# Kernel optimization log

Measured on AMD Instinct MI355X. Metric: run time of the kernel, lower is better.

## Reference

```python
import jax, jax.numpy as jnp
import numpy as np

B, LS, LL = 1024, 128, 2048
E, VOCAB = 16, 160000
NH, KD = 8, 6
LSH_DIM, TOPK = 16, 48
D_ITEM = 3 * E  # 48
EPS = 1e-3  # keras LayerNormalization default epsilon


def setup_inputs() -> dict:
    key = jax.random.key(0)
    ks = iter(jax.random.split(key, 64))
    def nk():
        return next(ks)
    def ids(shape):
        return jax.random.randint(nk(), shape, 0, VOCAB, dtype=jnp.int32)
    inp = {}
    for n in ['uid', 'utag1', 'utag2', 'utag3', 'utag4',
              'label_goods_ids', 'label_shop_ids', 'label_cate_ids']:
        inp[n] = ids((B,))
    for n in ['shortterm_goods_ids', 'shortterm_shop_ids', 'shortterm_cate_ids']:
        inp[n] = ids((B, LS))
    for n in ['longterm_goods_ids', 'longterm_shop_ids', 'longterm_cate_ids']:
        inp[n] = ids((B, LL))
    def rn(shape, s=0.05):
        return (jax.random.normal(nk(), shape) * s).astype(jnp.float32)
    inp['emb_table'] = rn((VOCAB, E))
    inp['H'] = rn((D_ITEM, LSH_DIM), 1.0)  # non-trainable random projection
    for p in ('s', 'l'):
        inp[p + 'Wq'] = rn((D_ITEM, NH, KD)); inp[p + 'bq'] = jnp.zeros((NH, KD), jnp.float32)
        inp[p + 'Wk'] = rn((D_ITEM, NH, KD)); inp[p + 'bk'] = jnp.zeros((NH, KD), jnp.float32)
        inp[p + 'Wv'] = rn((D_ITEM, NH, KD)); inp[p + 'bv'] = jnp.zeros((NH, KD), jnp.float32)
        inp[p + 'Wo'] = rn((NH, KD, D_ITEM)); inp[p + 'bo'] = jnp.zeros((D_ITEM,), jnp.float32)
    Din = D_ITEM + 5 * E + D_ITEM + D_ITEM  # 224
    inp['W1'] = rn((Din, 200)); inp['b1'] = jnp.zeros((200,), jnp.float32)
    inp['g1'] = jnp.ones((200,), jnp.float32); inp['be1'] = jnp.zeros((200,), jnp.float32)
    inp['W2'] = rn((200, 80)); inp['b2'] = jnp.zeros((80,), jnp.float32)
    inp['g2'] = jnp.ones((80,), jnp.float32); inp['be2'] = jnp.zeros((80,), jnp.float32)
    inp['W3'] = rn((80, 1)); inp['b3'] = jnp.zeros((1,), jnp.float32)
    return inp


def _ln(x, g, b):
    m = jnp.mean(x, axis=-1, keepdims=True)
    v = jnp.mean((x - m) ** 2, axis=-1, keepdims=True)
    return (x - m) * jax.lax.rsqrt(v + EPS) * g + b


def _mha(q, kv, mask3, Wq, bq, Wk, bk, Wv, bv, Wo, bo):
    # q: [B,1,D], kv: [B,K,D], mask3: [B,1,K] float (1=keep)
    qh = jnp.einsum('bqe,ehd->bqhd', q, Wq) + bq
    kh = jnp.einsum('bke,ehd->bkhd', kv, Wk) + bk
    vh = jnp.einsum('bke,ehd->bkhd', kv, Wv) + bv
    sc = jnp.einsum('bqhd,bkhd->bhqk', qh, kh) / jnp.sqrt(jnp.float32(KD))
    sc = sc + (1.0 - mask3[:, None, :, :]) * jnp.float32(-1e9)
    a = jax.nn.softmax(sc, axis=-1)
    o = jnp.einsum('bhqk,bkhd->bqhd', a, vh)
    return jnp.einsum('bqhd,hde->bqe', o, Wo) + bo


def reference(uid, utag1, utag2, utag3, utag4,
              label_goods_ids, label_shop_ids, label_cate_ids,
              shortterm_goods_ids, shortterm_shop_ids, shortterm_cate_ids,
              longterm_goods_ids, longterm_shop_ids, longterm_cate_ids,
              emb_table, H,
              sWq, sbq, sWk, sbk, sWv, sbv, sWo, sbo,
              lWq, lbq, lWk, lbk, lWv, lbv, lWo, lbo,
              W1, b1, g1, be1, W2, b2, g2, be2, W3, b3):
    short_mask = shortterm_goods_ids == 0  # padding_index == 0
    long_mask = longterm_goods_ids == 0

    def stack_embed(lst):
        X = jnp.stack([t if t.ndim == 2 else t[:, None] for t in lst], axis=2)  # [B,L,F]
        Xe = emb_table[X]  # [B,L,F,E]
        return Xe.reshape(Xe.shape[0], Xe.shape[1], -1)

    X_item = stack_embed([label_goods_ids, label_shop_ids, label_cate_ids])  # [B,1,48]
    X_user = stack_embed([uid, utag1, utag2, utag3, utag4])                  # [B,1,80]
    X_short = stack_embed([shortterm_goods_ids, shortterm_shop_ids, shortterm_cate_ids])  # [B,LS,48]
    X_long = stack_embed([longterm_goods_ids, longterm_shop_ids, longterm_cate_ids])      # [B,LL,48]

    # short-term interest
    slen = jnp.sum((~short_mask).astype(jnp.int32), axis=1)
    smask = (jnp.arange(LS)[None, :] < slen[:, None]).astype(jnp.float32)[:, None, :]
    short_int = _mha(X_item, X_short, smask, sWq, sbq, sWk, sbk, sWv, sbv, sWo, sbo)[:, 0]

    # long-term interest: LSH sign-hash hamming top-k retrieval
    series_codes = jnp.sign(jnp.einsum('ble,em->blm', X_long, H))  # [B,LL,16]
    item_codes = jnp.sign(jnp.einsum('ble,em->blm', X_item, H))    # [B,1,16]
    scores = jnp.sum((series_codes == item_codes).astype(jnp.float32), axis=-1)  # [B,LL]
    scores = jnp.where(long_mask, -jnp.inf, scores)
    _, idx = jax.lax.top_k(scores, TOPK)  # descending, padded entries last
    top_emb = jnp.take_along_axis(X_long, idx[:, :, None], axis=1)  # [B,TOPK,48]
    top_mask = jnp.take_along_axis(long_mask, idx, axis=1)
    llen = jnp.sum((~top_mask).astype(jnp.int32), axis=1)
    lmask = (jnp.arange(TOPK)[None, :] < llen[:, None]).astype(jnp.float32)[:, None, :]
    long_int = _mha(X_item, top_emb, lmask, lWq, lbq, lWk, lbk, lWv, lbv, lWo, lbo)[:, 0]

    x = jnp.concatenate([X_item[:, 0], X_user[:, 0], short_int, long_int], axis=1)  # [B,224]
    h1 = jax.nn.relu(_ln(x @ W1 + b1, g1, be1))
    h2 = jax.nn.relu(_ln(h1 @ W2 + b2, g2, be2))
    out = jax.nn.sigmoid(h2 @ W3 + b3)  # [B,1]
    return out
```

## Files before the change

kernel.cpp:

```cpp
#include <hip/hip_runtime.h>
#include <hip/hip_fp16.h>
#include <math.h>

#define BB 1024
#define LSx 128
#define LLx 2048
#define TOPKx 48
#define VOCABx 160000

__global__ __launch_bounds__(256) void k_partial(
    const float* __restrict__ emb, const float* __restrict__ Hm,
    __half* __restrict__ Ph)
{
  const int idx = blockIdx.x * 256 + threadIdx.x;
  if (idx >= VOCABx * 48) return;
  const int v = idx / 48;
  const int r = idx - v * 48;
  const int seg = r >> 4, m = r & 15;
  const float* er = emb + (size_t)v * 16;
  float a = 0.f;
  #pragma unroll
  for (int e = 0; e < 16; ++e) a += er[e] * Hm[(seg * 16 + e) * 16 + m];
  Ph[idx] = __float2half(a);
}

__global__ __launch_bounds__(512) void k_score_topk(
    const int* __restrict__ lg, const int* __restrict__ lsh, const int* __restrict__ lc,
    const int* __restrict__ ig, const int* __restrict__ ish, const int* __restrict__ ici,
    const float* __restrict__ emb, const float* __restrict__ Hm,
    const __half* __restrict__ Ph,
    int* __restrict__ sel)
{
  __shared__ int idsL[3 * LLx];
  __shared__ signed char scores[LLx];
  __shared__ float Xitem[48];
  __shared__ int icodeS[16];
  __shared__ int hist[18];
  __shared__ int cnt_above;
  __shared__ int wsum[8];
  const int b = blockIdx.x, tid = threadIdx.x;

  ((int4*)idsL)[tid]        = ((const int4*)(lg  + (size_t)b * LLx))[tid];
  ((int4*)idsL)[512 + tid]  = ((const int4*)(lsh + (size_t)b * LLx))[tid];
  ((int4*)idsL)[1024 + tid] = ((const int4*)(lc  + (size_t)b * LLx))[tid];
  if (tid < 48) {
    const int seg = tid >> 4, e = tid & 15;
    const int id = (seg == 0) ? ig[b] : (seg == 1) ? ish[b] : ici[b];
    Xitem[tid] = emb[(size_t)id * 16 + e];
  }
  if (tid < 18) hist[tid] = 0;
  if (tid == 0) cnt_above = 0;
  __syncthreads();
  if (tid < 16) {
    float dd = 0.f;
    for (int e = 0; e < 48; ++e) dd += Xitem[e] * Hm[e * 16 + tid];
    icodeS[tid] = (dd > 0.f) ? 1 : (dd < 0.f ? -1 : 0);
  }
  __syncthreads();

  const int l16 = tid & 15;
  const int grpw = (tid >> 4) & 3;
  const int grp32 = tid >> 4;
  const int myic = icodeS[l16];

  for (int r4 = 0; r4 < 64; r4 += 4) {
    int g_[4], s_[4], c_[4];
    #pragma unroll
    for (int u = 0; u < 4; ++u) {
      const int p = (r4 + u) * 32 + grp32;
      g_[u] = idsL[p]; s_[u] = idsL[LLx + p]; c_[u] = idsL[2 * LLx + p];
    }
    float d0[4], d1[4], d2[4];
    #pragma unroll
    for (int u = 0; u < 4; ++u) {
      d0[u] = __half2float(Ph[(size_t)g_[u] * 48 + l16]);
      d1[u] = __half2float(Ph[(size_t)s_[u] * 48 + 16 + l16]);
      d2[u] = __half2float(Ph[(size_t)c_[u] * 48 + 32 + l16]);
    }
    #pragma unroll
    for (int u = 0; u < 4; ++u) {
      const int p = (r4 + u) * 32 + grp32;
      const float d = (d0[u] + d1[u]) + d2[u];
      const int cs = (d > 0.f) ? 1 : (d < 0.f ? -1 : 0);
      const unsigned long long bal = __ballot(cs == myic);
      int sc = (int)__popcll((bal >> (16 * grpw)) & 0xFFFFull);
      if (g_[u] == 0) sc = -1;
      if (l16 == 0) {
        scores[p] = (signed char)sc;
        atomicAdd(&hist[sc + 1], 1);
      }
    }
  }
  __syncthreads();

  int above = 0, tval = -1, need = 0;
  for (int s = 16; s >= -1; --s) {
    const int c = hist[s + 1];
    if (above + c >= TOPKx) { tval = s; need = TOPKx - above; break; }
    above += c;
  }

  const int base_l = tid * 4;
  int myscore[4];
  #pragma unroll
  for (int j = 0; j < 4; ++j) myscore[j] = scores[base_l + j];
  int cnt = 0;
  #pragma unroll
  for (int j = 0; j < 4; ++j) cnt += (myscore[j] == tval) ? 1 : 0;
  int v = cnt;
  const int lane = tid & 63, wave = tid >> 6;
  #pragma unroll
  for (int o = 1; o < 64; o <<= 1) {
    const int u = __shfl_up(v, o, 64);
    if (lane >= o) v += u;
  }
  if (lane == 63) wsum[wave] = v;
  __syncthreads();
  int rank = v - cnt;
  for (int w = 0; w < wave; ++w) rank += wsum[w];

  #pragma unroll
  for (int j = 0; j < 4; ++j) {
    const int l = base_l + j;
    const int s = myscore[j];
    if (s > tval) {
      const int slot = atomicAdd(&cnt_above, 1);
      sel[b * TOPKx + slot] = l;
    } else if (s == tval) {
      if (rank < need) sel[b * TOPKx + above + rank] = l;
      ++rank;
    }
  }
}

__device__ __forceinline__ void kv_accum(
    const float* __restrict__ W, const float* __restrict__ bvec,
    int gid, int sid, int cid, const float* __restrict__ emb, float acc[48])
{
  #pragma unroll
  for (int j = 0; j < 48; ++j) acc[j] = bvec[j];
  const int ids3[3] = {gid, sid, cid};
  #pragma unroll
  for (int seg = 0; seg < 3; ++seg) {
    const float* row = emb + (size_t)ids3[seg] * 16;
    #pragma unroll
    for (int i4 = 0; i4 < 4; ++i4) {
      const float4 xv = ((const float4*)row)[i4];
      const float xs[4] = {xv.x, xv.y, xv.z, xv.w};
      #pragma unroll
      for (int c = 0; c < 4; ++c) {
        const int e = seg * 16 + i4 * 4 + c;
        const float* wr = W + e * 48;
        const float xe = xs[c];
        #pragma unroll
        for (int j = 0; j < 48; ++j) acc[j] += xe * wr[j];
      }
    }
  }
}

template<int K, int STRIDE, bool IS_LONG>
__global__ __launch_bounds__(256) void k_mha(
    const int* __restrict__ kg, const int* __restrict__ ks, const int* __restrict__ kc,
    const int* __restrict__ ig, const int* __restrict__ ish, const int* __restrict__ ici,
    const float* __restrict__ emb,
    const float* __restrict__ Wq, const float* __restrict__ bq,
    const float* __restrict__ Wk, const float* __restrict__ bk,
    const float* __restrict__ Wv, const float* __restrict__ bv,
    const float* __restrict__ Wo, const float* __restrict__ bo,
    const int* __restrict__ sel,
    float* __restrict__ outv)
{
  __shared__ float Xitem[48];
  __shared__ float qh[48];
  __shared__ __align__(16) float vhs[K][48];
  __shared__ float scs[8][K + 4];
  __shared__ float osm[48];
  __shared__ unsigned char validf[K];
  const int b = blockIdx.x, tid = threadIdx.x;
  const int role = tid >> 7;
  const int p = tid & 127;

  if (tid < 48) {
    const int seg = tid >> 4, e = tid & 15;
    const int id = (seg == 0) ? ig[b] : (seg == 1) ? ish[b] : ici[b];
    Xitem[tid] = emb[(size_t)id * 16 + e];
  }
  __syncthreads();
  if (tid < 48) {
    float a = bq[tid];
    for (int e = 0; e < 48; ++e) a += Xitem[e] * Wq[e * 48 + tid];
    qh[tid] = a;
  }

  int gid = 0, sid = 0, cid = 0;
  if (p < K) {
    const int pos = IS_LONG ? sel[b * TOPKx + p] : p;
    const size_t off = (size_t)b * STRIDE + pos;
    gid = kg[off]; sid = ks[off]; cid = kc[off];
  }
  const int nval = __syncthreads_count(role == 0 && p < K && gid != 0);

  if (p < K) {
    if (role == 0) {
      float acc[48];
      kv_accum(Wk, bk, gid, sid, cid, emb, acc);
      validf[p] = IS_LONG ? (unsigned char)(gid != 0) : (unsigned char)(p < nval);
      #pragma unroll
      for (int h = 0; h < 8; ++h) {
        float s = 0.f;
        #pragma unroll
        for (int d = 0; d < 6; ++d) s += qh[h * 6 + d] * acc[h * 6 + d];
        scs[h][p] = s * 0.40824829046386301637f;
      }
    } else {
      float acc[48];
      kv_accum(Wv, bv, gid, sid, cid, emb, acc);
      #pragma unroll
      for (int j = 0; j < 48; ++j) vhs[p][j] = acc[j];
    }
  }
  __syncthreads();

  if (tid < 128) {
    const int h = tid >> 4, l16 = tid & 15;
    float amax = -INFINITY;
    for (int k = l16; k < K; k += 16) if (validf[k]) amax = fmaxf(amax, scs[h][k]);
    #pragma unroll
    for (int m = 1; m < 16; m <<= 1) amax = fmaxf(amax, __shfl_xor(amax, m, 16));
    if (nval == 0) {
      for (int k = l16; k < K; k += 16) scs[h][k] = 1.0f / (float)K;
    } else {
      float ssum = 0.f;
      for (int k = l16; k < K; k += 16) {
        const float ev = validf[k] ? expf(scs[h][k] - amax) : 0.f;
        scs[h][k] = ev;
        ssum += ev;
      }
      #pragma unroll
      for (int m = 1; m < 16; m <<= 1) ssum += __shfl_xor(ssum, m, 16);
      const float inv = 1.0f / ssum;
      for (int k = l16; k < K; k += 16) scs[h][k] *= inv;
    }
  }
  __syncthreads();

  if (tid < 48) {
    const int h = tid / 6;
    float a = 0.f;
    for (int k = 0; k < K; ++k) a += scs[h][k] * vhs[k][tid];
    osm[tid] = a;
  }
  __syncthreads();
  if (tid < 48) {
    float r = bo[tid];
    for (int j = 0; j < 48; ++j) r += osm[j] * Wo[j * 48 + tid];
    outv[b * 48 + tid] = r;
  }
}

__device__ __forceinline__ float block_sum256(float v, float* red) {
  #pragma unroll
  for (int m = 32; m >= 1; m >>= 1) v += __shfl_xor(v, m, 64);
  const int lane = threadIdx.x & 63, wave = threadIdx.x >> 6;
  if (lane == 0) red[wave] = v;
  __syncthreads();
  const float t = red[0] + red[1] + red[2] + red[3];
  __syncthreads();
  return t;
}

__global__ __launch_bounds__(256) void k_mlp(
    const int* __restrict__ uid, const int* __restrict__ u1, const int* __restrict__ u2,
    const int* __restrict__ u3, const int* __restrict__ u4,
    const int* __restrict__ ig, const int* __restrict__ ish, const int* __restrict__ ici,
    const float* __restrict__ emb,
    const float* __restrict__ sint, const float* __restrict__ lint,
    const float* __restrict__ W1, const float* __restrict__ b1,
    const float* __restrict__ g1, const float* __restrict__ be1,
    const float* __restrict__ W2, const float* __restrict__ b2,
    const float* __restrict__ g2, const float* __restrict__ be2,
    const float* __restrict__ W3, const float* __restrict__ b3,
    float* __restrict__ out)
{
  __shared__ __align__(16) float x[224];
  __shared__ __align__(16) float h1[200];
  __shared__ float h2[80];
  __shared__ float red[4];
  const int b = blockIdx.x, tid = threadIdx.x;

  if (tid < 128) {
    const int e = tid & 15;
    int id;
    if (tid < 48) {
      const int seg = tid >> 4;
      id = (seg == 0) ? ig[b] : (seg == 1) ? ish[b] : ici[b];
    } else {
      const int f = (tid - 48) >> 4;
      id = (f == 0) ? uid[b] : (f == 1) ? u1[b] : (f == 2) ? u2[b] : (f == 3) ? u3[b] : u4[b];
    }
    x[tid] = emb[(size_t)id * 16 + e];
  } else if (tid < 176) {
    x[tid] = sint[b * 48 + (tid - 128)];
  } else if (tid < 224) {
    x[tid] = lint[b * 48 + (tid - 176)];
  }
  __syncthreads();

  float v = 0.f;
  if (tid < 200) {
    float a0 = b1[tid], a1 = 0.f, a2 = 0.f, a3 = 0.f;
    for (int i4 = 0; i4 < 56; ++i4) {
      const float4 xv = *(const float4*)(x + i4 * 4);
      const float* w = W1 + i4 * 4 * 200 + tid;
      a0 += xv.x * w[0];
      a1 += xv.y * w[200];
      a2 += xv.z * w[400];
      a3 += xv.w * w[600];
    }
    v = (a0 + a1) + (a2 + a3);
  }
  const float mean1 = block_sum256((tid < 200) ? v : 0.f, red) * (1.0f / 200.0f);
  const float dv = (tid < 200) ? (v - mean1) : 0.f;
  const float var1 = block_sum256(dv * dv, red) * (1.0f / 200.0f);
  if (tid < 200) {
    const float y = (v - mean1) * rsqrtf(var1 + 1e-3f) * g1[tid] + be1[tid];
    h1[tid] = fmaxf(y, 0.f);
  }
  __syncthreads();

  float v2 = 0.f;
  if (tid < 80) {
    float a0 = b2[tid], a1 = 0.f, a2 = 0.f, a3 = 0.f;
    for (int i4 = 0; i4 < 50; ++i4) {
      const float4 xv = *(const float4*)(h1 + i4 * 4);
      const float* w = W2 + i4 * 4 * 80 + tid;
      a0 += xv.x * w[0];
      a1 += xv.y * w[80];
      a2 += xv.z * w[160];
      a3 += xv.w * w[240];
    }
    v2 = (a0 + a1) + (a2 + a3);
  }
  const float mean2 = block_sum256((tid < 80) ? v2 : 0.f, red) * (1.0f / 80.0f);
  const float dv2 = (tid < 80) ? (v2 - mean2) : 0.f;
  const float var2 = block_sum256(dv2 * dv2, red) * (1.0f / 80.0f);
  if (tid < 80) {
    const float y = (v2 - mean2) * rsqrtf(var2 + 1e-3f) * g2[tid] + be2[tid];
    h2[tid] = fmaxf(y, 0.f);
  }
  __syncthreads();

  const float p = (tid < 80) ? h2[tid] * W3[tid] : 0.f;
  const float z = block_sum256(p, red);
  if (tid == 0) {
    out[b] = 1.0f / (1.0f + expf(-(z + b3[0])));
  }
}

extern "C" void kernel_launch(void* const* d_in, const int* in_sizes, int n_in,
                              void* d_out, int out_size, void* d_ws, size_t ws_size,
                              hipStream_t stream) {
  (void)in_sizes; (void)n_in; (void)out_size; (void)ws_size;
  const int* uid = (const int*)d_in[0];
  const int* u1  = (const int*)d_in[1];
  const int* u2  = (const int*)d_in[2];
  const int* u3  = (const int*)d_in[3];
  const int* u4  = (const int*)d_in[4];
  const int* ig  = (const int*)d_in[5];
  const int* ish = (const int*)d_in[6];
  const int* ici = (const int*)d_in[7];
  const int* sg  = (const int*)d_in[8];
  const int* ss  = (const int*)d_in[9];
  const int* scd = (const int*)d_in[10];
  const int* lg  = (const int*)d_in[11];
  const int* ls  = (const int*)d_in[12];
  const int* lcd = (const int*)d_in[13];
  const float* emb = (const float*)d_in[14];
  const float* Hm  = (const float*)d_in[15];
  const float* sWq = (const float*)d_in[16];
  const float* sbq = (const float*)d_in[17];
  const float* sWk = (const float*)d_in[18];
  const float* sbk = (const float*)d_in[19];
  const float* sWv = (const float*)d_in[20];
  const float* sbv = (const float*)d_in[21];
  const float* sWo = (const float*)d_in[22];
  const float* sbo = (const float*)d_in[23];
  const float* lWq = (const float*)d_in[24];
  const float* lbq = (const float*)d_in[25];
  const float* lWk = (const float*)d_in[26];
  const float* lbk = (const float*)d_in[27];
  const float* lWv = (const float*)d_in[28];
  const float* lbv = (const float*)d_in[29];
  const float* lWo = (const float*)d_in[30];
  const float* lbo = (const float*)d_in[31];
  const float* W1 = (const float*)d_in[32];
  const float* b1 = (const float*)d_in[33];
  const float* g1 = (const float*)d_in[34];
  const float* be1 = (const float*)d_in[35];
  const float* W2 = (const float*)d_in[36];
  const float* b2 = (const float*)d_in[37];
  const float* g2 = (const float*)d_in[38];
  const float* be2 = (const float*)d_in[39];
  const float* W3 = (const float*)d_in[40];
  const float* b3 = (const float*)d_in[41];
  float* out = (float*)d_out;

  int* sel = (int*)d_ws;
  float* sint = (float*)d_ws + BB * TOPKx;
  float* lint = sint + BB * 48;
  __half* Ph = (__half*)(lint + BB * 48);

  k_partial<<<dim3((VOCABx * 48 + 255) / 256), dim3(256), 0, stream>>>(emb, Hm, Ph);
  k_score_topk<<<dim3(BB), dim3(512), 0, stream>>>(lg, ls, lcd, ig, ish, ici, emb, Hm, Ph, sel);
  k_mha<128, 128, false><<<dim3(BB), dim3(256), 0, stream>>>(
      sg, ss, scd, ig, ish, ici, emb,
      sWq, sbq, sWk, sbk, sWv, sbv, sWo, sbo, (const int*)nullptr, sint);
  k_mha<48, 2048, true><<<dim3(BB), dim3(256), 0, stream>>>(
      lg, ls, lcd, ig, ish, ici, emb,
      lWq, lbq, lWk, lbk, lWv, lbv, lWo, lbo, sel, lint);
  k_mlp<<<dim3(BB), dim3(256), 0, stream>>>(
      uid, u1, u2, u3, u4, ig, ish, ici, emb,
      sint, lint, W1, b1, g1, be1, W2, b2, g2, be2, W3, b3, out);
}
```

Before: 342.5 us.

## Fuse score/top-k, long and short MHA into one kernel; vectorize partial

Merges the LSH scoring/top-k kernel, the long-term MHA and the short-term MHA into a single 2*B-block kernel. Long blocks keep selected indices and ids in shared memory instead of round-tripping through global memory, and short blocks run alongside them. K/V projection work is split across more threads with fewer accumulators each, and the score loop is unrolled 8-deep for more memory-level parallelism. The partial-projection kernel now has one thread per vocab row with vectorized half2/uint4 stores. The cost is heavier shared memory use and register pressure under launch_bounds(512,4), plus divergent block roles.

```diff
diff --git a/kernel.cpp b/kernel.cpp
--- a/kernel.cpp
+++ b/kernel.cpp
@@ -12,250 +12,372 @@
     const float* __restrict__ emb, const float* __restrict__ Hm,
     __half* __restrict__ Ph)
 {
-  const int idx = blockIdx.x * 256 + threadIdx.x;
-  if (idx >= VOCABx * 48) return;
-  const int v = idx / 48;
-  const int r = idx - v * 48;
-  const int seg = r >> 4, m = r & 15;
-  const float* er = emb + (size_t)v * 16;
-  float a = 0.f;
-  #pragma unroll
-  for (int e = 0; e < 16; ++e) a += er[e] * Hm[(seg * 16 + e) * 16 + m];
-  Ph[idx] = __float2half(a);
-}
-
-__global__ __launch_bounds__(512) void k_score_topk(
+  const int v = blockIdx.x * 256 + threadIdx.x;
+  if (v >= VOCABx) return;
+  const float4* er = (const float4*)(emb + (size_t)v * 16);
+  const float4 x0 = er[0], x1 = er[1], x2 = er[2], x3 = er[3];
+  const float x[16] = {x0.x, x0.y, x0.z, x0.w, x1.x, x1.y, x1.z, x1.w,
+                       x2.x, x2.y, x2.z, x2.w, x3.x, x3.y, x3.z, x3.w};
+  unsigned int packed[24];
+  #pragma unroll
+  for (int seg = 0; seg < 3; ++seg) {
+    #pragma unroll
+    for (int mp = 0; mp < 8; ++mp) {
+      float a0 = 0.f, a1 = 0.f;
+      #pragma unroll
+      for (int e = 0; e < 16; ++e) {
+        a0 += x[e] * Hm[(seg * 16 + e) * 16 + 2 * mp];
+        a1 += x[e] * Hm[(seg * 16 + e) * 16 + 2 * mp + 1];
+      }
+      const __half2 hp = __floats2half2_rn(a0, a1);
+      packed[seg * 8 + mp] = *(const unsigned int*)&hp;
+    }
+  }
+  uint4* dst = (uint4*)(Ph + (size_t)v * 48);
+  #pragma unroll
+  for (int q = 0; q < 6; ++q) {
+    uint4 o;
+    o.x = packed[q * 4 + 0]; o.y = packed[q * 4 + 1];
+    o.z = packed[q * 4 + 2]; o.w = packed[q * 4 + 3];
+    dst[q] = o;
+  }
+}
+
+__device__ __forceinline__ void kv12(
+    const float* __restrict__ W, const float* __restrict__ bvec, int j0,
+    int gid, int sid, int cid, const float* __restrict__ emb, float acc[12])
+{
+  #pragma unroll
+  for (int j = 0; j < 12; ++j) acc[j] = bvec[j0 + j];
+  const int ids3[3] = {gid, sid, cid};
+  #pragma unroll
+  for (int seg = 0; seg < 3; ++seg) {
+    const float* row = emb + (size_t)ids3[seg] * 16;
+    #pragma unroll
+    for (int i4 = 0; i4 < 4; ++i4) {
+      const float4 xv = ((const float4*)row)[i4];
+      const float xs[4] = {xv.x, xv.y, xv.z, xv.w};
+      #pragma unroll
+      for (int c = 0; c < 4; ++c) {
+        const float* wr = W + (seg * 16 + i4 * 4 + c) * 48 + j0;
+        const float xe = xs[c];
+        #pragma unroll
+        for (int j = 0; j < 12; ++j) acc[j] += xe * wr[j];
+      }
+    }
+  }
+}
+
+__device__ __forceinline__ void kv24(
+    const float* __restrict__ W, const float* __restrict__ bvec, int j0,
+    int gid, int sid, int cid, const float* __restrict__ emb, float acc[24])
+{
+  #pragma unroll
+  for (int j = 0; j < 24; ++j) acc[j] = bvec[j0 + j];
+  const int ids3[3] = {gid, sid, cid};
+  #pragma unroll
+  for (int seg = 0; seg < 3; ++seg) {
+    const float* row = emb + (size_t)ids3[seg] * 16;
+    #pragma unroll
+    for (int i4 = 0; i4 < 4; ++i4) {
+      const float4 xv = ((const float4*)row)[i4];
+      const float xs[4] = {xv.x, xv.y, xv.z, xv.w};
+      #pragma unroll
+      for (int c = 0; c < 4; ++c) {
+        const float* wr = W + (seg * 16 + i4 * 4 + c) * 48 + j0;
+        const float xe = xs[c];
+        #pragma unroll
+        for (int j = 0; j < 24; ++j) acc[j] += xe * wr[j];
+      }
+    }
+  }
+}
+
+__global__ __launch_bounds__(512, 4) void k_main(
     const int* __restrict__ lg, const int* __restrict__ lsh, const int* __restrict__ lc,
+    const int* __restrict__ sg, const int* __restrict__ ss, const int* __restrict__ scd,
     const int* __restrict__ ig, const int* __restrict__ ish, const int* __restrict__ ici,
     const float* __restrict__ emb, const float* __restrict__ Hm,
     const __half* __restrict__ Ph,
-    int* __restrict__ sel)
+    const float* __restrict__ sWq, const float* __restrict__ sbq,
+    const float* __restrict__ sWk, const float* __restrict__ sbk,
+    const float* __restrict__ sWv, const float* __restrict__ sbv,
+    const float* __restrict__ sWo, const float* __restrict__ sbo,
+    const float* __restrict__ lWq, const float* __restrict__ lbq,
+    const float* __restrict__ lWk, const float* __restrict__ lbk,
+    const float* __restrict__ lWv, const float* __restrict__ lbv,
+    const float* __restrict__ lWo, const float* __restrict__ lbo,
+    float* __restrict__ sint, float* __restrict__ lint)
 {
-  __shared__ int idsL[3 * LLx];
-  __shared__ signed char scores[LLx];
-  __shared__ float Xitem[48];
-  __shared__ int icodeS[16];
-  __shared__ int hist[18];
-  __shared__ int cnt_above;
-  __shared__ int wsum[8];
-  const int b = blockIdx.x, tid = threadIdx.x;
-
-  ((int4*)idsL)[tid]        = ((const int4*)(lg  + (size_t)b * LLx))[tid];
-  ((int4*)idsL)[512 + tid]  = ((const int4*)(lsh + (size_t)b * LLx))[tid];
-  ((int4*)idsL)[1024 + tid] = ((const int4*)(lc  + (size_t)b * LLx))[tid];
-  if (tid < 48) {
-    const int seg = tid >> 4, e = tid & 15;
-    const int id = (seg == 0) ? ig[b] : (seg == 1) ? ish[b] : ici[b];
-    Xitem[tid] = emb[(size_t)id * 16 + e];
-  }
-  if (tid < 18) hist[tid] = 0;
-  if (tid == 0) cnt_above = 0;
-  __syncthreads();
-  if (tid < 16) {
-    float dd = 0.f;
-    for (int e = 0; e < 48; ++e) dd += Xitem[e] * Hm[e * 16 + tid];
-    icodeS[tid] = (dd > 0.f) ? 1 : (dd < 0.f ? -1 : 0);
-  }
-  __syncthreads();
-
-  const int l16 = tid & 15;
-  const int grpw = (tid >> 4) & 3;
-  const int grp32 = tid >> 4;
-  const int myic = icodeS[l16];
-
-  for (int r4 = 0; r4 < 64; r4 += 4) {
-    int g_[4], s_[4], c_[4];
-    #pragma unroll
-    for (int u = 0; u < 4; ++u) {
-      const int p = (r4 + u) * 32 + grp32;
-      g_[u] = idsL[p]; s_[u] = idsL[LLx + p]; c_[u] = idsL[2 * LLx + p];
-    }
-    float d0[4], d1[4], d2[4];
-    #pragma unroll
-    for (int u = 0; u < 4; ++u) {
-      d0[u] = __half2float(Ph[(size_t)g_[u] * 48 + l16]);
-      d1[u] = __half2float(Ph[(size_t)s_[u] * 48 + 16 + l16]);
-      d2[u] = __half2float(Ph[(size_t)c_[u] * 48 + 32 + l16]);
-    }
-    #pragma unroll
-    for (int u = 0; u < 4; ++u) {
-      const int p = (r4 + u) * 32 + grp32;
-      const float d = (d0[u] + d1[u]) + d2[u];
-      const int cs = (d > 0.f) ? 1 : (d < 0.f ? -1 : 0);
-      const unsigned long long bal = __ballot(cs == myic);
-      int sc = (int)__popcll((bal >> (16 * grpw)) & 0xFFFFull);
-      if (g_[u] == 0) sc = -1;
-      if (l16 == 0) {
-        scores[p] = (signed char)sc;
-        atomicAdd(&hist[sc + 1], 1);
-      }
-    }
-  }
-  __syncthreads();
-
-  int above = 0, tval = -1, need = 0;
-  for (int s = 16; s >= -1; --s) {
-    const int c = hist[s + 1];
-    if (above + c >= TOPKx) { tval = s; need = TOPKx - above; break; }
-    above += c;
-  }
-
-  const int base_l = tid * 4;
-  int myscore[4];
-  #pragma unroll
-  for (int j = 0; j < 4; ++j) myscore[j] = scores[base_l + j];
-  int cnt = 0;
-  #pragma unroll
-  for (int j = 0; j < 4; ++j) cnt += (myscore[j] == tval) ? 1 : 0;
-  int v = cnt;
+  __shared__ __align__(16) char pool[38912];
+  const int bid = blockIdx.x, tid = threadIdx.x;
   const int lane = tid & 63, wave = tid >> 6;
-  #pragma unroll
-  for (int o = 1; o < 64; o <<= 1) {
-    const int u = __shfl_up(v, o, 64);
-    if (lane >= o) v += u;
-  }
-  if (lane == 63) wsum[wave] = v;
-  __syncthreads();
-  int rank = v - cnt;
-  for (int w = 0; w < wave; ++w) rank += wsum[w];
-
-  #pragma unroll
-  for (int j = 0; j < 4; ++j) {
-    const int l = base_l + j;
-    const int s = myscore[j];
-    if (s > tval) {
-      const int slot = atomicAdd(&cnt_above, 1);
-      sel[b * TOPKx + slot] = l;
-    } else if (s == tval) {
-      if (rank < need) sel[b * TOPKx + above + rank] = l;
-      ++rank;
-    }
-  }
-}
-
-__device__ __forceinline__ void kv_accum(
-    const float* __restrict__ W, const float* __restrict__ bvec,
-    int gid, int sid, int cid, const float* __restrict__ emb, float acc[48])
-{
-  #pragma unroll
-  for (int j = 0; j < 48; ++j) acc[j] = bvec[j];
-  const int ids3[3] = {gid, sid, cid};
-  #pragma unroll
-  for (int seg = 0; seg < 3; ++seg) {
-    const float* row = emb + (size_t)ids3[seg] * 16;
-    #pragma unroll
-    for (int i4 = 0; i4 < 4; ++i4) {
-      const float4 xv = ((const float4*)row)[i4];
-      const float xs[4] = {xv.x, xv.y, xv.z, xv.w};
-      #pragma unroll
-      for (int c = 0; c < 4; ++c) {
-        const int e = seg * 16 + i4 * 4 + c;
-        const float* wr = W + e * 48;
-        const float xe = xs[c];
-        #pragma unroll
-        for (int j = 0; j < 48; ++j) acc[j] += xe * wr[j];
-      }
-    }
-  }
-}
-
-template<int K, int STRIDE, bool IS_LONG>
-__global__ __launch_bounds__(256) void k_mha(
-    const int* __restrict__ kg, const int* __restrict__ ks, const int* __restrict__ kc,
-    const int* __restrict__ ig, const int* __restrict__ ish, const int* __restrict__ ici,
-    const float* __restrict__ emb,
-    const float* __restrict__ Wq, const float* __restrict__ bq,
-    const float* __restrict__ Wk, const float* __restrict__ bk,
-    const float* __restrict__ Wv, const float* __restrict__ bv,
-    const float* __restrict__ Wo, const float* __restrict__ bo,
-    const int* __restrict__ sel,
-    float* __restrict__ outv)
-{
-  __shared__ float Xitem[48];
-  __shared__ float qh[48];
-  __shared__ __align__(16) float vhs[K][48];
-  __shared__ float scs[8][K + 4];
-  __shared__ float osm[48];
-  __shared__ unsigned char validf[K];
-  const int b = blockIdx.x, tid = threadIdx.x;
-  const int role = tid >> 7;
-  const int p = tid & 127;
-
-  if (tid < 48) {
-    const int seg = tid >> 4, e = tid & 15;
-    const int id = (seg == 0) ? ig[b] : (seg == 1) ? ish[b] : ici[b];
-    Xitem[tid] = emb[(size_t)id * 16 + e];
-  }
-  __syncthreads();
-  if (tid < 48) {
-    float a = bq[tid];
-    for (int e = 0; e < 48; ++e) a += Xitem[e] * Wq[e * 48 + tid];
-    qh[tid] = a;
-  }
-
-  int gid = 0, sid = 0, cid = 0;
-  if (p < K) {
-    const int pos = IS_LONG ? sel[b * TOPKx + p] : p;
-    const size_t off = (size_t)b * STRIDE + pos;
-    gid = kg[off]; sid = ks[off]; cid = kc[off];
-  }
-  const int nval = __syncthreads_count(role == 0 && p < K && gid != 0);
-
-  if (p < K) {
+
+  if (bid < BB) {
+    const int b = bid;
+    int* idsL = (int*)pool;
+    signed char* scores = (signed char*)(pool + 24576);
+    int* selL = (int*)(pool + 26624);
+    int* hist = (int*)(pool + 26816);
+    int* icodeS = (int*)(pool + 26896);
+    int* wsum = (int*)(pool + 26960);
+    int* cnt_above = (int*)(pool + 26992);
+    float* Xitem = (float*)(pool + 27008);
+    float* vhs = (float*)(pool + 27200);
+    float* scs = (float*)(pool + 36608);
+    float* qh = (float*)(pool + 38272);
+    float* osm = (float*)(pool + 38464);
+    unsigned char* validf = (unsigned char*)(pool + 38656);
+
+    ((int4*)idsL)[tid]        = ((const int4*)(lg  + (size_t)b * LLx))[tid];
+    ((int4*)idsL)[512 + tid]  = ((const int4*)(lsh + (size_t)b * LLx))[tid];
+    ((int4*)idsL)[1024 + tid] = ((const int4*)(lc  + (size_t)b * LLx))[tid];
+    if (tid < 48) {
+      const int seg = tid >> 4, e = tid & 15;
+      const int id = (seg == 0) ? ig[b] : (seg == 1) ? ish[b] : ici[b];
+      Xitem[tid] = emb[(size_t)id * 16 + e];
+    }
+    if (tid < 18) hist[tid] = 0;
+    if (tid == 0) *cnt_above = 0;
+    __syncthreads();
+    if (tid < 16) {
+      float dd = 0.f;
+      for (int e = 0; e < 48; ++e) dd += Xitem[e] * Hm[e * 16 + tid];
+      icodeS[tid] = (dd > 0.f) ? 1 : (dd < 0.f ? -1 : 0);
+    }
+    __syncthreads();
+
+    const int l16 = tid & 15;
+    const int grpw = (tid >> 4) & 3;
+    const int grp32 = tid >> 4;
+    const int myic = icodeS[l16];
+
+    for (int r8 = 0; r8 < 64; r8 += 8) {
+      int g_[8], s_[8], c_[8];
+      #pragma unroll
+      for (int u = 0; u < 8; ++u) {
+        const int p = (r8 + u) * 32 + grp32;
+        g_[u] = idsL[p]; s_[u] = idsL[LLx + p]; c_[u] = idsL[2 * LLx + p];
+      }
+      float d0[8], d1[8], d2[8];
+      #pragma unroll
+      for (int u = 0; u < 8; ++u) {
+        d0[u] = __half2float(Ph[(size_t)g_[u] * 48 + l16]);
+        d1[u] = __half2float(Ph[(size_t)s_[u] * 48 + 16 + l16]);
+        d2[u] = __half2float(Ph[(size_t)c_[u] * 48 + 32 + l16]);
+      }
+      #pragma unroll
+      for (int u = 0; u < 8; ++u) {
+        const int p = (r8 + u) * 32 + grp32;
+        const float d = (d0[u] + d1[u]) + d2[u];
+        const int cs = (d > 0.f) ? 1 : (d < 0.f ? -1 : 0);
+        const unsigned long long bal = __ballot(cs == myic);
+        int sc = (int)__popcll((bal >> (16 * grpw)) & 0xFFFFull);
+        if (g_[u] == 0) sc = -1;
+        if (l16 == 0) {
+          scores[p] = (signed char)sc;
+          atomicAdd(&hist[sc + 1], 1);
+        }
+      }
+    }
+    __syncthreads();
+
+    int above = 0, tval = -1, need = 0;
+    for (int s = 16; s >= -1; --s) {
+      const int c = hist[s + 1];
+      if (above + c >= TOPKx) { tval = s; need = TOPKx - above; break; }
+      above += c;
+    }
+
+    const int base_l = tid * 4;
+    int myscore[4];
+    #pragma unroll
+    for (int j = 0; j < 4; ++j) myscore[j] = scores[base_l + j];
+    int cnt = 0;
+    #pragma unroll
+    for (int j = 0; j < 4; ++j) cnt += (myscore[j] == tval) ? 1 : 0;
+    int v = cnt;
+    #pragma unroll
+    for (int o = 1; o < 64; o <<= 1) {
+      const int u = __shfl_up(v, o, 64);
+      if (lane >= o) v += u;
+    }
+    if (lane == 63) wsum[wave] = v;
+    __syncthreads();
+    int rank = v - cnt;
+    for (int w = 0; w < wave; ++w) rank += wsum[w];
+
+    #pragma unroll
+    for (int j = 0; j < 4; ++j) {
+      const int l = base_l + j;
+      const int s = myscore[j];
+      if (s > tval) {
+        const int slot = atomicAdd(cnt_above, 1);
+        selL[slot] = l;
+      } else if (s == tval) {
+        if (rank < need) selL[above + rank] = l;
+        ++rank;
+      }
+    }
+    __syncthreads();
+
+    const int role = wave >> 2;
+    const int jq = wave & 3;
+    const int p = lane;
+    const bool act = (lane < 48);
+    int gid = 0, sid = 0, cid = 0;
+    if (act) {
+      const int pos = selL[p];
+      gid = idsL[pos]; sid = idsL[LLx + pos]; cid = idsL[2 * LLx + pos];
+      if (tid < 48) validf[p] = (unsigned char)(gid != 0);
+    }
+    if (tid < 48) {
+      float a = lbq[tid];
+      for (int e = 0; e < 48; ++e) a += Xitem[e] * lWq[e * 48 + tid];
+      qh[tid] = a;
+    }
+    const int j0 = __builtin_amdgcn_readfirstlane(jq * 12);
+    float acc[12];
+    if (role == 0) kv12(lWk, lbk, j0, gid, sid, cid, emb, acc);
+    else           kv12(lWv, lbv, j0, gid, sid, cid, emb, acc);
+    const int nval = __syncthreads_count(tid < 48 && gid != 0);
+
+    if (act) {
+      if (role == 0) {
+        #pragma unroll
+        for (int hh = 0; hh < 2; ++hh) {
+          const int h = jq * 2 + hh;
+          float s = 0.f;
+          #pragma unroll
+          for (int d = 0; d < 6; ++d) s += qh[h * 6 + d] * acc[hh * 6 + d];
+          scs[h * 52 + p] = s * 0.40824829046386301637f;
+        }
+      } else {
+        #pragma unroll
+        for (int j = 0; j < 12; ++j) vhs[p * 49 + j0 + j] = acc[j];
+      }
+    }
+    __syncthreads();
+
+    if (tid < 128) {
+      const int h = tid >> 4, l16b = tid & 15;
+      float amax = -INFINITY;
+      for (int k = l16b; k < TOPKx; k += 16) if (validf[k]) amax = fmaxf(amax, scs[h * 52 + k]);
+      #pragma unroll
+      for (int m = 1; m < 16; m <<= 1) amax = fmaxf(amax, __shfl_xor(amax, m, 16));
+      if (nval == 0) {
+        for (int k = l16b; k < TOPKx; k += 16) scs[h * 52 + k] = 1.0f / (float)TOPKx;
+      } else {
+        float ssum = 0.f;
+        for (int k = l16b; k < TOPKx; k += 16) {
+          const float ev = validf[k] ? expf(scs[h * 52 + k] - amax) : 0.f;
+          scs[h * 52 + k] = ev;
+          ssum += ev;
+        }
+        #pragma unroll
+        for (int m = 1; m < 16; m <<= 1) ssum += __shfl_xor(ssum, m, 16);
+        const float inv = 1.0f / ssum;
+        for (int k = l16b; k < TOPKx; k += 16) scs[h * 52 + k] *= inv;
+      }
+    }
+    __syncthreads();
+
+    if (tid < 48) {
+      const int h = tid / 6;
+      float a = 0.f;
+      for (int k = 0; k < TOPKx; ++k) a += scs[h * 52 + k] * vhs[k * 49 + tid];
+      osm[tid] = a;
+    }
+    __syncthreads();
+    if (tid < 48) {
+      float r = lbo[tid];
+      for (int j = 0; j < 48; ++j) r += osm[j] * lWo[j * 48 + tid];
+      lint[b * 48 + tid] = r;
+    }
+  } else {
+    const int b = bid - BB;
+    float* Xitem = (float*)pool;
+    float* qh = (float*)(pool + 192);
+    float* vhs = (float*)(pool + 384);
+    float* scs = (float*)(pool + 25472);
+    float* osm = (float*)(pool + 29696);
+    unsigned char* validf = (unsigned char*)(pool + 29888);
+
+    if (tid < 48) {
+      const int seg = tid >> 4, e = tid & 15;
+      const int id = (seg == 0) ? ig[b] : (seg == 1) ? ish[b] : ici[b];
+      Xitem[tid] = emb[(size_t)id * 16 + e];
+    }
+    __syncthreads();
+    if (tid < 48) {
+      float a = sbq[tid];
+      for (int e = 0; e < 48; ++e) a += Xitem[e] * sWq[e * 48 + tid];
+      qh[tid] = a;
+    }
+
+    const int role = wave >> 2;
+    const int jh = (wave >> 1) & 1;
+    const int p = ((wave & 1) << 6) | lane;
+    const size_t off = (size_t)b * LSx + p;
+    const int gid = sg[off], sid = ss[off], cid = scd[off];
+    const int nval = __syncthreads_count(tid < 128 && gid != 0);
+    if (tid < 128) validf[p] = (unsigned char)(p < nval);
+
+    const int j0 = __builtin_amdgcn_readfirstlane(jh * 24);
+    float acc[24];
+    if (role == 0) kv24(sWk, sbk, j0, gid, sid, cid, emb, acc);
+    else           kv24(sWv, sbv, j0, gid, sid, cid, emb, acc);
+
     if (role == 0) {
-      float acc[48];
-      kv_accum(Wk, bk, gid, sid, cid, emb, acc);
-      validf[p] = IS_LONG ? (unsigned char)(gid != 0) : (unsigned char)(p < nval);
-      #pragma unroll
-      for (int h = 0; h < 8; ++h) {
+      #pragma unroll
+      for (int hh = 0; hh < 4; ++hh) {
+        const int h = jh * 4 + hh;
         float s = 0.f;
         #pragma unroll
-        for (int d = 0; d < 6; ++d) s += qh[h * 6 + d] * acc[h * 6 + d];
-        scs[h][p] = s * 0.40824829046386301637f;
+        for (int d = 0; d < 6; ++d) s += qh[h * 6 + d] * acc[hh * 6 + d];
+        scs[h * 132 + p] = s * 0.40824829046386301637f;
       }
     } else {
-      float acc[48];
-      kv_accum(Wv, bv, gid, sid, cid, emb, acc);
-      #pragma unroll
-      for (int j = 0; j < 48; ++j) vhs[p][j] = acc[j];
-    }
-  }
-  __syncthreads();
-
-  if (tid < 128) {
-    const int h = tid >> 4, l16 = tid & 15;
-    float amax = -INFINITY;
-    for (int k = l16; k < K; k += 16) if (validf[k]) amax = fmaxf(amax, scs[h][k]);
-    #pragma unroll
-    for (int m = 1; m < 16; m <<= 1) amax = fmaxf(amax, __shfl_xor(amax, m, 16));
-    if (nval == 0) {
-      for (int k = l16; k < K; k += 16) scs[h][k] = 1.0f / (float)K;
-    } else {
-      float ssum = 0.f;
-      for (int k = l16; k < K; k += 16) {
-        const float ev = validf[k] ? expf(scs[h][k] - amax) : 0.f;
-        scs[h][k] = ev;
-        ssum += ev;
-      }
-      #pragma unroll
-      for (int m = 1; m < 16; m <<= 1) ssum += __shfl_xor(ssum, m, 16);
-      const float inv = 1.0f / ssum;
-      for (int k = l16; k < K; k += 16) scs[h][k] *= inv;
-    }
-  }
-  __syncthreads();
-
-  if (tid < 48) {
-    const int h = tid / 6;
-    float a = 0.f;
-    for (int k = 0; k < K; ++k) a += scs[h][k] * vhs[k][tid];
-    osm[tid] = a;
-  }
-  __syncthreads();
-  if (tid < 48) {
-    float r = bo[tid];
-    for (int j = 0; j < 48; ++j) r += osm[j] * Wo[j * 48 + tid];
-    outv[b * 48 + tid] = r;
+      #pragma unroll
+      for (int j = 0; j < 24; ++j) vhs[p * 49 + j0 + j] = acc[j];
+    }
+    __syncthreads();
+
+    if (tid < 128) {
+      const int h = tid >> 4, l16b = tid & 15;
+      float amax = -INFINITY;
+      for (int k = l16b; k < LSx; k += 16) if (validf[k]) amax = fmaxf(amax, scs[h * 132 + k]);
+      #pragma unroll
+      for (int m = 1; m < 16; m <<= 1) amax = fmaxf(amax, __shfl_xor(amax, m, 16));
+      if (nval == 0) {
+        for (int k = l16b; k < LSx; k += 16) scs[h * 132 + k] = 1.0f / (float)LSx;
+      } else {
+        float ssum = 0.f;
+        for (int k = l16b; k < LSx; k += 16) {
+          const float ev = validf[k] ? expf(scs[h * 132 + k] - amax) : 0.f;
+          scs[h * 132 + k] = ev;
+          ssum += ev;
+        }
+        #pragma unroll
+        for (int m = 1; m < 16; m <<= 1) ssum += __shfl_xor(ssum, m, 16);
+        const float inv = 1.0f / ssum;
+        for (int k = l16b; k < LSx; k += 16) scs[h * 132 + k] *= inv;
+      }
+    }
+    __syncthreads();
+
+    if (tid < 48) {
+      const int h = tid / 6;
+      float a = 0.f;
+      for (int k = 0; k < LSx; ++k) a += scs[h * 132 + k] * vhs[k * 49 + tid];
+      osm[tid] = a;
+    }
+    __syncthreads();
+    if (tid < 48) {
+      float r = sbo[tid];
+      for (int j = 0; j < 48; ++j) r += osm[j] * sWo[j * 48 + tid];
+      sint[b * 48 + tid] = r;
+    }
   }
 }
 
@@ -406,19 +528,16 @@
   const float* b3 = (const float*)d_in[41];
   float* out = (float*)d_out;
 
-  int* sel = (int*)d_ws;
-  float* sint = (float*)d_ws + BB * TOPKx;
+  float* sint = (float*)d_ws;
   float* lint = sint + BB * 48;
   __half* Ph = (__half*)(lint + BB * 48);
 
-  k_partial<<<dim3((VOCABx * 48 + 255) / 256), dim3(256), 0, stream>>>(emb, Hm, Ph);
-  k_score_topk<<<dim3(BB), dim3(512), 0, stream>>>(lg, ls, lcd, ig, ish, ici, emb, Hm, Ph, sel);
-  k_mha<128, 128, false><<<dim3(BB), dim3(256), 0, stream>>>(
-      sg, ss, scd, ig, ish, ici, emb,
-      sWq, sbq, sWk, sbk, sWv, sbv, sWo, sbo, (const int*)nullptr, sint);
-  k_mha<48, 2048, true><<<dim3(BB), dim3(256), 0, stream>>>(
-      lg, ls, lcd, ig, ish, ici, emb,
-      lWq, lbq, lWk, lbk, lWv, lbv, lWo, lbo, sel, lint);
+  k_partial<<<dim3((VOCABx + 255) / 256), dim3(256), 0, stream>>>(emb, Hm, Ph);
+  k_main<<<dim3(2 * BB), dim3(512), 0, stream>>>(
+      lg, ls, lcd, sg, ss, scd, ig, ish, ici, emb, Hm, Ph,
+      sWq, sbq, sWk, sbk, sWv, sbv, sWo, sbo,
+      lWq, lbq, lWk, lbk, lWv, lbv, lWo, lbo,
+      sint, lint);
   k_mlp<<<dim3(BB), dim3(256), 0, stream>>>(
       uid, u1, u2, u3, u4, ig, ish, ici, emb,
       sint, lint, W1, b1, g1, be1, W2, b2, g2, be2, W3, b3, out);
```

Measured after the change: 886.6 us. 2.59x slower.
